# Performance work log

Hardware: AMD Instinct MI355X
Metric: run time of the kernel (lower is better)

## Reference

```python
import jax, jax.numpy as jnp
import numpy as np

B, C, H, W = 64, 384, 32, 32
N_EXPERTS = 128
EPS = 1e-12  # F.normalize default eps


def setup_inputs() -> dict:
    key = jax.random.key(0)
    k1, k2, k3, k4 = jax.random.split(key, 4)
    x = jax.random.normal(k1, (B, C, H, W), dtype=jnp.float32)
    # nn.init.normal_(phi, std=1/dim**0.5)
    phi = jax.random.normal(k2, (C, N_EXPERTS, 1), dtype=jnp.float32) / jnp.sqrt(jnp.float32(C))
    scale = jnp.ones((1,), dtype=jnp.float32)
    # per-expert 1x1 conv == dense dim->dim; stacked weights [n, out, in] and bias [n, out]
    w_exp = jax.random.normal(k3, (N_EXPERTS, C, C), dtype=jnp.float32) / jnp.sqrt(jnp.float32(C))
    b_exp = jax.random.normal(k4, (N_EXPERTS, C), dtype=jnp.float32) * 0.01
    return {"x": x, "phi": phi, "scale": scale, "w_exp": w_exp, "b_exp": b_exp}


def reference(x, phi, scale, w_exp, b_exp):
    Bb, Cc, Hh, Ww = x.shape
    M = Hh * Ww
    t = x.reshape(Bb, Cc, M).transpose(0, 2, 1)  # [B, M, D] tokens
    # sec 2.3 normalization
    xn = t / jnp.maximum(jnp.linalg.norm(t, axis=2, keepdims=True), EPS)
    phin = scale * phi / jnp.maximum(jnp.linalg.norm(phi, axis=0, keepdims=True), EPS)
    logits = jnp.einsum('bmd,dnp->bmnp', xn, phin)  # [B, M, N, 1]
    d = jax.nn.softmax(logits, axis=1)  # dispatch: softmax over tokens
    # combine: softmax over (expert, slot) jointly
    c = jax.nn.softmax(logits.reshape(Bb, M, -1), axis=-1).reshape(logits.shape)
    xs = jnp.einsum('bmd,bmnp->bnpd', xn, d)[:, :, 0, :]  # [B, N, D] slot inputs
    # per-expert 1x1 conv applied to its single slot
    ys = jnp.einsum('bnd,nod->bno', xs, w_exp) + b_exp  # [B, N, D]
    y = jnp.einsum('bnd,bmn->bmd', ys, c[..., 0])  # [B, M, D]
    return y.transpose(0, 2, 1).reshape(Bb, Cc, Hh, Ww)
```

## Files before the change

### kernel.cpp

```cpp
#include <hip/hip_runtime.h>
#include <hip/hip_bf16.h>
#include <math.h>

#define B_ 64
#define C_ 384
#define M_ 1024
#define N_ 128
#define EPSV 1e-12f

typedef __attribute__((ext_vector_type(8))) short bf16x8;
typedef __attribute__((ext_vector_type(4))) float f32x4;

__device__ __forceinline__ short f2b(float f) {
    unsigned u = __float_as_uint(f);
    unsigned r = (u + 0x7FFFu + ((u >> 16) & 1u)) >> 16;
    return (short)r;
}

template <int R>
__device__ __forceinline__ void stage32(const short* gbase, size_t ld, short* lds, int tid) {
    int w = tid >> 6, l = tid & 63;
#pragma unroll
    for (int q = 0; q < (R >> 6); ++q) {
        int c = ((q << 2) + w) * 64 + l;
        int row = c >> 2;
        int kq = (c & 3) ^ ((row >> 1) & 3);
        const short* src = gbase + (size_t)row * ld + (kq << 3);
        short* dst = lds + (((q << 2) + w) << 9);
        __builtin_amdgcn_global_load_lds((const __attribute__((address_space(1))) void*)src,
                                         (__attribute__((address_space(3))) void*)dst, 16, 0, 0);
    }
}

__device__ __forceinline__ bf16x8 fragLd(const short* lds, int row, int g) {
    int kq = g ^ ((row >> 1) & 3);
    return *reinterpret_cast<const bf16x8*>(lds + row * 32 + (kq << 3));
}

#define MFMA16(a, b, c) __builtin_amdgcn_mfma_f32_16x16x32_bf16(a, b, c, 0, 0, 0)

__global__ void k_phin(const float* __restrict__ phi, const float* __restrict__ scale,
                       short* __restrict__ phin_bf) {
    int n = blockIdx.x, t = threadIdx.x;
    float v[6];
    float ss = 0.f;
#pragma unroll
    for (int i = 0; i < 6; ++i) {
        int d = t + 64 * i;
        float u = phi[d * N_ + n];
        v[i] = u; ss += u * u;
    }
#pragma unroll
    for (int off = 32; off; off >>= 1) ss += __shfl_down(ss, off);
    ss = __shfl(ss, 0);
    float s = scale[0] / fmaxf(sqrtf(ss), EPSV);
#pragma unroll
    for (int i = 0; i < 6; ++i) phin_bf[n * C_ + t + 64 * i] = f2b(v[i] * s);
}

__global__ void k_cvt(const float* __restrict__ in, short* __restrict__ out, int n8) {
    for (int i = blockIdx.x * 256 + threadIdx.x; i < n8; i += gridDim.x * 256) {
        float4 a = reinterpret_cast<const float4*>(in)[2 * i];
        float4 b = reinterpret_cast<const float4*>(in)[2 * i + 1];
        bf16x8 r;
        r[0] = f2b(a.x); r[1] = f2b(a.y); r[2] = f2b(a.z); r[3] = f2b(a.w);
        r[4] = f2b(b.x); r[5] = f2b(b.y); r[6] = f2b(b.z); r[7] = f2b(b.w);
        reinterpret_cast<bf16x8*>(out)[i] = r;
    }
}

__global__ void k_xn(const float* __restrict__ x, short* __restrict__ xdm) {
    int b = blockIdx.y;
    int m = blockIdx.x * 256 + threadIdx.x;
    const float* p = x + (size_t)b * C_ * M_ + m;
    float ss = 0.f;
#pragma unroll 4
    for (int c = 0; c < C_; ++c) { float u = p[(size_t)c * M_]; ss += u * u; }
    float inv = 1.0f / fmaxf(sqrtf(ss), EPSV);
    short* q = xdm + (size_t)b * C_ * M_ + m;
#pragma unroll 4
    for (int c = 0; c < C_; ++c) q[(size_t)c * M_] = f2b(p[(size_t)c * M_] * inv);
}

__global__ __launch_bounds__(256) void k_tr(const short* __restrict__ in, short* __restrict__ out,
                                            int RI, int CI) {
    __shared__ __align__(16) short t[64][68];
    int b = blockIdx.z, c0 = blockIdx.x * 64, r0 = blockIdx.y * 64;
    int tid = threadIdx.x;
    int cq = (tid & 15) * 4, rp = tid >> 4;
    const size_t ibase = (size_t)b * RI * CI;
#pragma unroll
    for (int p = 0; p < 4; ++p) {
        int r = r0 + p * 16 + rp;
        short4 v = *reinterpret_cast<const short4*>(in + ibase + (size_t)r * CI + c0 + cq);
        t[p * 16 + rp][cq + 0] = v.x; t[p * 16 + rp][cq + 1] = v.y;
        t[p * 16 + rp][cq + 2] = v.z; t[p * 16 + rp][cq + 3] = v.w;
    }
    __syncthreads();
    const size_t obase = (size_t)b * CI * RI;
#pragma unroll
    for (int p = 0; p < 4; ++p) {
        int c = c0 + p * 16 + rp;
        short4 v;
        v.x = t[cq + 0][p * 16 + rp]; v.y = t[cq + 1][p * 16 + rp];
        v.z = t[cq + 2][p * 16 + rp]; v.w = t[cq + 3][p * 16 + rp];
        *reinterpret_cast<short4*>(out + obase + (size_t)c * RI + r0 + cq) = v;
    }
}

__global__ __launch_bounds__(256) void k_glogits(const short* __restrict__ phin_bf,
                                                 const short* __restrict__ xmd,
                                                 float* __restrict__ L) {
    __shared__ __align__(16) short lA[4096];
    __shared__ __align__(16) short lB[4096];
    int tid = threadIdx.x, b = blockIdx.z, m0 = blockIdx.x * 128;
    int w = tid >> 6, wr = w >> 1, wc = w & 1, l = tid & 63, g = l >> 4, lr = l & 15;
    f32x4 acc[4][4];
#pragma unroll
    for (int i = 0; i < 4; ++i)
#pragma unroll
        for (int j = 0; j < 4; ++j) acc[i][j] = (f32x4)(0.f);
    for (int k0 = 0; k0 < C_; k0 += 32) {
        stage32<128>(phin_bf + k0, C_, lA, tid);
        stage32<128>(xmd + ((size_t)(b * M_ + m0)) * C_ + k0, C_, lB, tid);
        __syncthreads();
        bf16x8 af[4], bf[4];
#pragma unroll
        for (int i = 0; i < 4; ++i) af[i] = fragLd(lA, wr * 64 + i * 16 + lr, g);
#pragma unroll
        for (int j = 0; j < 4; ++j) bf[j] = fragLd(lB, wc * 64 + j * 16 + lr, g);
#pragma unroll
        for (int i = 0; i < 4; ++i)
#pragma unroll
            for (int j = 0; j < 4; ++j) acc[i][j] = MFMA16(af[i], bf[j], acc[i][j]);
        __syncthreads();
    }
#pragma unroll
    for (int i = 0; i < 4; ++i)
#pragma unroll
        for (int j = 0; j < 4; ++j)
#pragma unroll
            for (int rr = 0; rr < 4; ++rr) {
                int n = wr * 64 + i * 16 + g * 4 + rr;
                int m = m0 + wc * 64 + j * 16 + lr;
                L[((size_t)b * N_ + n) * M_ + m] = acc[i][j][rr];
            }
}

__global__ __launch_bounds__(256) void k_dstats(const float* __restrict__ L,
                                                float* __restrict__ dmax, float* __restrict__ dsum) {
    __shared__ float red[256];
    int bn = blockIdx.x;
    const float* row = L + (size_t)bn * M_;
    int t = threadIdx.x;
    float v[4];
    float mx = -3.4e38f;
#pragma unroll
    for (int i = 0; i < 4; ++i) { v[i] = row[t + 256 * i]; mx = fmaxf(mx, v[i]); }
    red[t] = mx; __syncthreads();
    for (int s = 128; s > 0; s >>= 1) { if (t < s) red[t] = fmaxf(red[t], red[t + s]); __syncthreads(); }
    float MX = red[0]; __syncthreads();
    float se = 0.f;
#pragma unroll
    for (int i = 0; i < 4; ++i) se += expf(v[i] - MX);
    red[t] = se; __syncthreads();
    for (int s = 128; s > 0; s >>= 1) { if (t < s) red[t] += red[t + s]; __syncthreads(); }
    if (t == 0) { dmax[bn] = MX; dsum[bn] = red[0]; }
}

__global__ void k_cstats(const float* __restrict__ L, float* __restrict__ cmax,
                         float* __restrict__ csum) {
    int idx = blockIdx.x * 256 + threadIdx.x;
    int b = idx >> 10, m = idx & (M_ - 1);
    const float* p = L + (size_t)b * N_ * M_ + m;
    float mx = -3.4e38f;
#pragma unroll 4
    for (int n = 0; n < N_; ++n) mx = fmaxf(mx, p[(size_t)n * M_]);
    float s = 0.f;
#pragma unroll 4
    for (int n = 0; n < N_; ++n) s += expf(p[(size_t)n * M_] - mx);
    cmax[idx] = mx; csum[idx] = s;
}

__global__ __launch_bounds__(256) void k_weights(const float* __restrict__ L,
                                                 const float* __restrict__ dmax, const float* __restrict__ dsum,
                                                 const float* __restrict__ cmax, const float* __restrict__ csum,
                                                 short* __restrict__ Dbf, short* __restrict__ Ct) {
    __shared__ __align__(16) short t[64][68];
    int b = blockIdx.z, n0 = blockIdx.y * 64, m0 = blockIdx.x * 64;
    int tid = threadIdx.x;
    int col = tid & 63, rp = tid >> 6;
    float cm = cmax[b * M_ + m0 + col];
    float rcs = 1.0f / csum[b * M_ + m0 + col];
#pragma unroll 4
    for (int rr = 0; rr < 16; ++rr) {
        int row = rr * 4 + rp;
        int n = n0 + row;
        float lv = L[((size_t)b * N_ + n) * M_ + m0 + col];
        float dv = expf(lv - dmax[b * N_ + n]) * (1.0f / dsum[b * N_ + n]);
        Dbf[((size_t)b * N_ + n) * M_ + m0 + col] = f2b(dv);
        t[row][col] = f2b(expf(lv - cm) * rcs);
    }
    __syncthreads();
    int cq = (tid & 15) * 4, rp2 = tid >> 4;
#pragma unroll
    for (int p = 0; p < 4; ++p) {
        int m = m0 + p * 16 + rp2;
        short4 v;
        v.x = t[cq + 0][p * 16 + rp2]; v.y = t[cq + 1][p * 16 + rp2];
        v.z = t[cq + 2][p * 16 + rp2]; v.w = t[cq + 3][p * 16 + rp2];
        *reinterpret_cast<short4*>(Ct + ((size_t)b * M_ + m) * N_ + n0 + cq) = v;
    }
}

__global__ __launch_bounds__(256) void k_gxs(const short* __restrict__ Dbf,
                                             const short* __restrict__ xdm,
                                             short* __restrict__ xs_bf) {
    __shared__ __align__(16) short lA[2048];
    __shared__ __align__(16) short lB[4096];
    int tid = threadIdx.x, b = blockIdx.z, n0 = blockIdx.y * 64, d0 = blockIdx.x * 128;
    int w = tid >> 6, l = tid & 63, g = l >> 4, lr = l & 15;
    f32x4 acc[4][2];
#pragma unroll
    for (int i = 0; i < 4; ++i)
#pragma unroll
        for (int j = 0; j < 2; ++j) acc[i][j] = (f32x4)(0.f);
    for (int k0 = 0; k0 < M_; k0 += 32) {
        stage32<64>(Dbf + ((size_t)(b * N_ + n0)) * M_ + k0, M_, lA, tid);
        stage32<128>(xdm + ((size_t)(b * C_ + d0)) * M_ + k0, M_, lB, tid);
        __syncthreads();
        bf16x8 af[4], bf[2];
#pragma unroll
        for (int i = 0; i < 4; ++i) af[i] = fragLd(lA, i * 16 + lr, g);
#pragma unroll
        for (int j = 0; j < 2; ++j) bf[j] = fragLd(lB, w * 32 + j * 16 + lr, g);
#pragma unroll
        for (int i = 0; i < 4; ++i)
#pragma unroll
            for (int j = 0; j < 2; ++j) acc[i][j] = MFMA16(af[i], bf[j], acc[i][j]);
        __syncthreads();
    }
#pragma unroll
    for (int i = 0; i < 4; ++i)
#pragma unroll
        for (int j = 0; j < 2; ++j)
#pragma unroll
            for (int rr = 0; rr < 4; ++rr) {
                int n = n0 + i * 16 + g * 4 + rr;
                int d = d0 + w * 32 + j * 16 + lr;
                xs_bf[((size_t)b * N_ + n) * C_ + d] = f2b(acc[i][j][rr]);
            }
}

__global__ __launch_bounds__(256) void k_gys(const short* __restrict__ xs_bf,
                                             const short* __restrict__ wbf,
                                             const float* __restrict__ b_exp,
                                             short* __restrict__ ys_bf) {
    __shared__ __align__(16) short lA[2048];
    __shared__ __align__(16) short lB[4096];
    int tid = threadIdx.x, n = blockIdx.y, o0 = blockIdx.x * 128;
    int w = tid >> 6, l = tid & 63, g = l >> 4, lr = l & 15;
    f32x4 acc[4][2];
#pragma unroll
    for (int i = 0; i < 4; ++i)
#pragma unroll
        for (int j = 0; j < 2; ++j) acc[i][j] = (f32x4)(0.f);
    for (int k0 = 0; k0 < C_; k0 += 32) {
        stage32<64>(xs_bf + (size_t)n * C_ + k0, (size_t)N_ * C_, lA, tid);
        stage32<128>(wbf + ((size_t)n * C_ + o0) * C_ + k0, C_, lB, tid);
        __syncthreads();
        bf16x8 af[4], bf[2];
#pragma unroll
        for (int i = 0; i < 4; ++i) af[i] = fragLd(lA, i * 16 + lr, g);
#pragma unroll
        for (int j = 0; j < 2; ++j) bf[j] = fragLd(lB, w * 32 + j * 16 + lr, g);
#pragma unroll
        for (int i = 0; i < 4; ++i)
#pragma unroll
            for (int j = 0; j < 2; ++j) acc[i][j] = MFMA16(af[i], bf[j], acc[i][j]);
        __syncthreads();
    }
#pragma unroll
    for (int i = 0; i < 4; ++i)
#pragma unroll
        for (int j = 0; j < 2; ++j)
#pragma unroll
            for (int rr = 0; rr < 4; ++rr) {
                int bb = i * 16 + g * 4 + rr;
                int o = o0 + w * 32 + j * 16 + lr;
                float v = acc[i][j][rr] + b_exp[n * C_ + o];
                ys_bf[((size_t)bb * N_ + n) * C_ + o] = f2b(v);
            }
}

__global__ __launch_bounds__(256) void k_gy(const short* __restrict__ ysT,
                                            const short* __restrict__ Ct,
                                            float* __restrict__ out) {
    __shared__ __align__(16) short lA[4096];
    __shared__ __align__(16) short lB[4096];
    int tid = threadIdx.x, b = blockIdx.z, d0 = blockIdx.y * 128, m0 = blockIdx.x * 128;
    int w = tid >> 6, wr = w >> 1, wc = w & 1, l = tid & 63, g = l >> 4, lr = l & 15;
    f32x4 acc[4][4];
#pragma unroll
    for (int i = 0; i < 4; ++i)
#pragma unroll
        for (int j = 0; j < 4; ++j) acc[i][j] = (f32x4)(0.f);
    for (int k0 = 0; k0 < N_; k0 += 32) {
        stage32<128>(ysT + ((size_t)(b * C_ + d0)) * N_ + k0, N_, lA, tid);
        stage32<128>(Ct + ((size_t)(b * M_ + m0)) * N_ + k0, N_, lB, tid);
        __syncthreads();
        bf16x8 af[4], bf[4];
#pragma unroll
        for (int i = 0; i < 4; ++i) af[i] = fragLd(lA, wr * 64 + i * 16 + lr, g);
#pragma unroll
        for (int j = 0; j < 4; ++j) bf[j] = fragLd(lB, wc * 64 + j * 16 + lr, g);
#pragma unroll
        for (int i = 0; i < 4; ++i)
#pragma unroll
            for (int j = 0; j < 4; ++j) acc[i][j] = MFMA16(af[i], bf[j], acc[i][j]);
        __syncthreads();
    }
#pragma unroll
    for (int i = 0; i < 4; ++i)
#pragma unroll
        for (int j = 0; j < 4; ++j)
#pragma unroll
            for (int rr = 0; rr < 4; ++rr) {
                int d = d0 + wr * 64 + i * 16 + g * 4 + rr;
                int m = m0 + wc * 64 + j * 16 + lr;
                out[((size_t)b * C_ + d) * M_ + m] = acc[i][j][rr];
            }
}

extern "C" void kernel_launch(void* const* d_in, const int* in_sizes, int n_in,
                              void* d_out, int out_size, void* d_ws, size_t ws_size,
                              hipStream_t stream) {
    const float* x     = (const float*)d_in[0];
    const float* phi   = (const float*)d_in[1];
    const float* scale = (const float*)d_in[2];
    const float* w_exp = (const float*)d_in[3];
    const float* b_exp = (const float*)d_in[4];
    float* out = (float*)d_out;

    char* w = (char*)d_ws;
    float* L     = (float*)(w + 0);
    float* dmax  = (float*)(w + 33554432);
    float* dsum  = (float*)(w + 33587200);
    float* cmax  = (float*)(w + 33619968);
    float* csum  = (float*)(w + 33882112);
    short* phin  = (short*)(w + 34144256);
    short* wbf   = (short*)(w + 34242560);
    short* xdm   = (short*)(w + 71991296);
    short* xmd   = (short*)(w + 122322944);
    short* Dbf   = (short*)(w + 172654592);
    short* Ct    = (short*)(w + 189431808);
    short* xs_bf = xmd;
    short* ys_bf = xmd + 3145728;
    short* ysT   = xmd + 6291456;

    if (ws_size < 206209024) return;

    k_phin<<<dim3(128), dim3(64), 0, stream>>>(phi, scale, phin);
    k_cvt<<<dim3(2048), dim3(256), 0, stream>>>(w_exp, wbf, N_ * C_ * C_ / 8);
    k_xn<<<dim3(4, 64), dim3(256), 0, stream>>>(x, xdm);
    k_tr<<<dim3(16, 6, 64), dim3(256), 0, stream>>>(xdm, xmd, C_, M_);
    k_glogits<<<dim3(8, 1, 64), dim3(256), 0, stream>>>(phin, xmd, L);
    k_dstats<<<dim3(8192), dim3(256), 0, stream>>>(L, dmax, dsum);
    k_cstats<<<dim3(256), dim3(256), 0, stream>>>(L, cmax, csum);
    k_weights<<<dim3(16, 2, 64), dim3(256), 0, stream>>>(L, dmax, dsum, cmax, csum, Dbf, Ct);
    k_gxs<<<dim3(3, 2, 64), dim3(256), 0, stream>>>(Dbf, xdm, xs_bf);
    k_gys<<<dim3(3, 128), dim3(256), 0, stream>>>(xs_bf, wbf, b_exp, ys_bf);
    k_tr<<<dim3(6, 2, 64), dim3(256), 0, stream>>>(ys_bf, ysT, N_, C_);
    k_gy<<<dim3(8, 3, 64), dim3(256), 0, stream>>>(ysT, Ct, out);
}
```

Baseline: 466.9 us.

## Fuse x normalization with transpose and convert expert weights inside GEMM

Replaces the separate normalize kernel and bf16 transpose kernel with one kernel that computes per-token norms using vectorized loads and writes both the channel-major and the token-major bf16 layouts through an LDS tile. It also drops the standalone fp32-to-bf16 conversion pass over the expert weights. The per-expert GEMM now loads fp32 weights directly and converts them while staging into LDS with the same swizzle. This removes two launches and a full write and read of the converted weight tensor, at the cost of reading fp32 weights, which is twice the bytes, inside the GEMM. x is also read twice within the fused kernel.

```diff
diff --git a/kernel.cpp b/kernel.cpp
--- a/kernel.cpp
+++ b/kernel.cpp
@@ -58,28 +58,59 @@
     for (int i = 0; i < 6; ++i) phin_bf[n * C_ + t + 64 * i] = f2b(v[i] * s);
 }
 
-__global__ void k_cvt(const float* __restrict__ in, short* __restrict__ out, int n8) {
-    for (int i = blockIdx.x * 256 + threadIdx.x; i < n8; i += gridDim.x * 256) {
-        float4 a = reinterpret_cast<const float4*>(in)[2 * i];
-        float4 b = reinterpret_cast<const float4*>(in)[2 * i + 1];
-        bf16x8 r;
-        r[0] = f2b(a.x); r[1] = f2b(a.y); r[2] = f2b(a.z); r[3] = f2b(a.w);
-        r[4] = f2b(b.x); r[5] = f2b(b.y); r[6] = f2b(b.z); r[7] = f2b(b.w);
-        reinterpret_cast<bf16x8*>(out)[i] = r;
-    }
-}
-
-__global__ void k_xn(const float* __restrict__ x, short* __restrict__ xdm) {
-    int b = blockIdx.y;
-    int m = blockIdx.x * 256 + threadIdx.x;
-    const float* p = x + (size_t)b * C_ * M_ + m;
-    float ss = 0.f;
-#pragma unroll 4
-    for (int c = 0; c < C_; ++c) { float u = p[(size_t)c * M_]; ss += u * u; }
-    float inv = 1.0f / fmaxf(sqrtf(ss), EPSV);
-    short* q = xdm + (size_t)b * C_ * M_ + m;
-#pragma unroll 4
-    for (int c = 0; c < C_; ++c) q[(size_t)c * M_] = f2b(p[(size_t)c * M_] * inv);
+__global__ __launch_bounds__(256) void k_xnt(const float* __restrict__ x,
+                                             short* __restrict__ xdm,
+                                             short* __restrict__ xmd) {
+    __shared__ float ssred[16][64];
+    __shared__ float invs[64];
+    __shared__ __align__(16) short tr[64][68];
+    int b = blockIdx.y, m0 = blockIdx.x * 64;
+    int tid = threadIdx.x;
+    int mq = tid & 15, cp = tid >> 4;
+    const float* xb = x + (size_t)b * C_ * M_ + m0;
+    float ss0 = 0.f, ss1 = 0.f, ss2 = 0.f, ss3 = 0.f;
+#pragma unroll
+    for (int i = 0; i < 24; ++i) {
+        int c = cp * 24 + i;
+        float4 v = *reinterpret_cast<const float4*>(xb + (size_t)c * M_ + mq * 4);
+        ss0 += v.x * v.x; ss1 += v.y * v.y; ss2 += v.z * v.z; ss3 += v.w * v.w;
+    }
+    ssred[cp][mq * 4 + 0] = ss0; ssred[cp][mq * 4 + 1] = ss1;
+    ssred[cp][mq * 4 + 2] = ss2; ssred[cp][mq * 4 + 3] = ss3;
+    __syncthreads();
+    if (tid < 64) {
+        float s = 0.f;
+#pragma unroll
+        for (int k = 0; k < 16; ++k) s += ssred[k][tid];
+        invs[tid] = 1.0f / fmaxf(sqrtf(s), EPSV);
+    }
+    __syncthreads();
+    float inv0 = invs[mq * 4 + 0], inv1 = invs[mq * 4 + 1];
+    float inv2 = invs[mq * 4 + 2], inv3 = invs[mq * 4 + 3];
+#pragma unroll
+    for (int p = 0; p < 6; ++p) {
+#pragma unroll
+        for (int i = 0; i < 4; ++i) {
+            int cl = i * 16 + cp;
+            int c = p * 64 + cl;
+            float4 v = *reinterpret_cast<const float4*>(xb + (size_t)c * M_ + mq * 4);
+            short4 o;
+            o.x = f2b(v.x * inv0); o.y = f2b(v.y * inv1);
+            o.z = f2b(v.z * inv2); o.w = f2b(v.w * inv3);
+            *reinterpret_cast<short4*>(xdm + ((size_t)b * C_ + c) * M_ + m0 + mq * 4) = o;
+            *reinterpret_cast<short4*>(&tr[cl][mq * 4]) = o;
+        }
+        __syncthreads();
+#pragma unroll
+        for (int q = 0; q < 4; ++q) {
+            int m = q * 16 + cp;
+            short4 v;
+            v.x = tr[mq * 4 + 0][m]; v.y = tr[mq * 4 + 1][m];
+            v.z = tr[mq * 4 + 2][m]; v.w = tr[mq * 4 + 3][m];
+            *reinterpret_cast<short4*>(xmd + ((size_t)b * M_ + m0 + m) * C_ + p * 64 + mq * 4) = v;
+        }
+        __syncthreads();
+    }
 }
 
 __global__ __launch_bounds__(256) void k_tr(const short* __restrict__ in, short* __restrict__ out,
@@ -253,7 +284,7 @@
 }
 
 __global__ __launch_bounds__(256) void k_gys(const short* __restrict__ xs_bf,
-                                             const short* __restrict__ wbf,
+                                             const float* __restrict__ w_exp,
                                              const float* __restrict__ b_exp,
                                              short* __restrict__ ys_bf) {
     __shared__ __align__(16) short lA[2048];
@@ -267,7 +298,19 @@
         for (int j = 0; j < 2; ++j) acc[i][j] = (f32x4)(0.f);
     for (int k0 = 0; k0 < C_; k0 += 32) {
         stage32<64>(xs_bf + (size_t)n * C_ + k0, (size_t)N_ * C_, lA, tid);
-        stage32<128>(wbf + ((size_t)n * C_ + o0) * C_ + k0, C_, lB, tid);
+#pragma unroll
+        for (int h = 0; h < 2; ++h) {
+            int cc = h * 256 + tid;
+            int row = cc >> 2, kq = cc & 3;
+            const float* src = w_exp + ((size_t)n * C_ + o0 + row) * C_ + k0 + kq * 8;
+            float4 a = *reinterpret_cast<const float4*>(src);
+            float4 bq = *reinterpret_cast<const float4*>(src + 4);
+            bf16x8 r;
+            r[0] = f2b(a.x); r[1] = f2b(a.y); r[2] = f2b(a.z); r[3] = f2b(a.w);
+            r[4] = f2b(bq.x); r[5] = f2b(bq.y); r[6] = f2b(bq.z); r[7] = f2b(bq.w);
+            int slot = kq ^ ((row >> 1) & 3);
+            *reinterpret_cast<bf16x8*>(lB + row * 32 + slot * 8) = r;
+        }
         __syncthreads();
         bf16x8 af[4], bf[2];
 #pragma unroll
@@ -349,27 +392,24 @@
     float* cmax  = (float*)(w + 33619968);
     float* csum  = (float*)(w + 33882112);
     short* phin  = (short*)(w + 34144256);
-    short* wbf   = (short*)(w + 34242560);
-    short* xdm   = (short*)(w + 71991296);
-    short* xmd   = (short*)(w + 122322944);
-    short* Dbf   = (short*)(w + 172654592);
-    short* Ct    = (short*)(w + 189431808);
+    short* xdm   = (short*)(w + 34242560);
+    short* xmd   = (short*)(w + 84574208);
+    short* Dbf   = (short*)(w + 134905856);
+    short* Ct    = (short*)(w + 151683072);
     short* xs_bf = xmd;
     short* ys_bf = xmd + 3145728;
     short* ysT   = xmd + 6291456;
 
-    if (ws_size < 206209024) return;
+    if (ws_size < 168460288) return;
 
     k_phin<<<dim3(128), dim3(64), 0, stream>>>(phi, scale, phin);
-    k_cvt<<<dim3(2048), dim3(256), 0, stream>>>(w_exp, wbf, N_ * C_ * C_ / 8);
-    k_xn<<<dim3(4, 64), dim3(256), 0, stream>>>(x, xdm);
-    k_tr<<<dim3(16, 6, 64), dim3(256), 0, stream>>>(xdm, xmd, C_, M_);
+    k_xnt<<<dim3(16, 64), dim3(256), 0, stream>>>(x, xdm, xmd);
     k_glogits<<<dim3(8, 1, 64), dim3(256), 0, stream>>>(phin, xmd, L);
     k_dstats<<<dim3(8192), dim3(256), 0, stream>>>(L, dmax, dsum);
     k_cstats<<<dim3(256), dim3(256), 0, stream>>>(L, cmax, csum);
     k_weights<<<dim3(16, 2, 64), dim3(256), 0, stream>>>(L, dmax, dsum, cmax, csum, Dbf, Ct);
     k_gxs<<<dim3(3, 2, 64), dim3(256), 0, stream>>>(Dbf, xdm, xs_bf);
-    k_gys<<<dim3(3, 128), dim3(256), 0, stream>>>(xs_bf, wbf, b_exp, ys_bf);
+    k_gys<<<dim3(3, 128), dim3(256), 0, stream>>>(xs_bf, w_exp, b_exp, ys_bf);
     k_tr<<<dim3(6, 2, 64), dim3(256), 0, stream>>>(ys_bf, ysT, N_, C_);
     k_gy<<<dim3(8, 3, 64), dim3(256), 0, stream>>>(ysT, Ct, out);
 }
```

After: 395.4 us. 15.3% less time.
